# Kernel tuning notes

Hardware: AMD Instinct MI355X
Metric: run time of the kernel (lower is better)

The kernel has to match this reference:

```python
import jax, jax.numpy as jnp
import numpy as np

# ---- Cl(3,0) Cayley table: blade order [1, e1, e2, e3, e12, e13, e23, e123] ----
_IDX2BM = [0, 1, 2, 4, 3, 5, 6, 7]
_BM2IDX = {b: i for i, b in enumerate(_IDX2BM)}

def _blade_mul(i, j):
    a, b = _IDX2BM[i], _IDX2BM[j]
    s, aa = 0, a >> 1
    while aa:
        s += bin(aa & b).count('1')
        aa >>= 1
    return _BM2IDX[a ^ b], (-1) ** s

_pairs = [(i, j) + _blade_mul(i, j) for i in range(8) for j in range(8) if i != j]
_pairs = [(i, j, k, s) for (i, j, k, s) in _pairs if k != i and k != j]
SRC_I = np.array([p[0] for p in _pairs])  # (42,)
SRC_J = np.array([p[1] for p in _pairs])
TGT   = np.array([p[2] for p in _pairs])
SIGN  = np.array([p[3] for p in _pairs], dtype=np.float32)

ROPE_THETA = 10000.0


def _rope_tables(T, D, dtype):
    inv_freq = 1.0 / (ROPE_THETA ** (jnp.arange(0, D, 2, dtype=jnp.float32) / D))
    freqs = jnp.arange(T, dtype=jnp.float32)[:, None] * inv_freq[None, :]  # (T, D/2)
    emb = jnp.concatenate([freqs, freqs], axis=-1)  # (T, D)
    return jnp.cos(emb).astype(dtype), jnp.sin(emb).astype(dtype)


def _rotate_half(x):
    x1, x2 = jnp.split(x, 2, axis=-1)
    return jnp.concatenate([-x2, x1], axis=-1)


def setup_inputs() -> dict:
    key = jax.random.key(0)
    k1, k2, k3 = jax.random.split(key, 3)
    B, T, N, D = 2, 2048, 8, 128
    d_model = N * D
    mv = jax.random.normal(k1, (B, T, N, D), dtype=jnp.float32)
    # nn.Linear weights, stored as (in, out) for x @ W; scaled like default init
    W_qkv = jax.random.normal(k2, (d_model, 3 * d_model), dtype=jnp.float32) / np.sqrt(d_model)
    W_o = jax.random.normal(k3, (d_model, d_model), dtype=jnp.float32) / np.sqrt(d_model)
    alpha = jnp.ones((8, 8), dtype=jnp.float32) * 0.01  # cayley_mix_init_scale
    return {"mv": mv, "W_qkv": W_qkv, "W_o": W_o, "alpha": alpha}


def reference(mv, W_qkv, W_o, alpha):
    B, T, N, D = mv.shape
    x_flat = mv.reshape(B, T, N * D)
    qkv = (x_flat @ W_qkv).reshape(B, T, 3, N, D)
    q, k, v = qkv[:, :, 0], qkv[:, :, 1], qkv[:, :, 2]  # (B, T, N, D)

    cos, sin = _rope_tables(T, D, mv.dtype)  # (T, D)
    cos = cos[None, :, None, :]
    sin = sin[None, :, None, :]
    q = q * cos + _rotate_half(q) * sin
    k = k * cos + _rotate_half(k) * sin

    # (B, N, T, D)
    q = q.transpose(0, 2, 1, 3)
    k = k.transpose(0, 2, 1, 3)
    v = v.transpose(0, 2, 1, 3)

    scale = 1.0 / jnp.sqrt(jnp.asarray(D, dtype=mv.dtype))
    scores = jnp.einsum('bntd,bnsd->bnts', q, k) * scale  # (B, N, T, T)
    causal = jnp.tril(jnp.ones((T, T), dtype=bool))
    scores = jnp.where(causal[None, None], scores, -jnp.inf)
    attn = jax.nn.softmax(scores, axis=-1)
    out = jnp.einsum('bnts,bnsd->bntd', attn, v)  # (B, N, T, D)

    out = out.transpose(0, 2, 1, 3).reshape(B, T, N * D)
    out = (out @ W_o).reshape(B, T, N, D)

    # Cayley cross-blade mixing
    si, sj, tgt = jnp.asarray(SRC_I), jnp.asarray(SRC_J), jnp.asarray(TGT)
    pair_w = alpha[si, sj] * jnp.asarray(SIGN)  # (42,)
    contrib = out[:, :, si, :] * out[:, :, sj, :] * pair_w[None, None, :, None]
    mixed = jnp.zeros_like(out).at[:, :, tgt, :].add(contrib)
    return out + mixed
```

## Files before the change

kernel.cpp:

```cpp
#include <hip/hip_runtime.h>
#include <stdint.h>


typedef __attribute__((ext_vector_type(8)))  __bf16 bf16x8;
typedef __attribute__((ext_vector_type(4)))  float  f32x4;

__device__ __forceinline__ uint16_t f2bf(float f) {
    uint32_t u = __float_as_uint(f);
    u += 0x7FFFu + ((u >> 16) & 1u);
    return (uint16_t)(u >> 16);
}
__device__ __forceinline__ float bf2f(uint16_t h) {
    return __uint_as_float(((uint32_t)h) << 16);
}

__device__ __forceinline__ void gload_lds16(const void* g, void* l) {
    __builtin_amdgcn_global_load_lds(
        (__attribute__((address_space(1))) void*)g,
        (__attribute__((address_space(3))) void*)l, 16, 0, 0);
}

__global__ __launch_bounds__(256) void k_cast(const float* __restrict__ in,
                                              uint16_t* __restrict__ out, int n) {
    int i = blockIdx.x * 256 + threadIdx.x;
    if (i * 4 >= n) return;
    float4 v = ((const float4*)in)[i];
    ushort4 o = make_ushort4(f2bf(v.x), f2bf(v.y), f2bf(v.z), f2bf(v.w));
    ((ushort4*)out)[i] = o;
}

__global__ __launch_bounds__(256) void k_wtrans(const float* __restrict__ W,
                                                uint16_t* __restrict__ Wt,
                                                int K, int N) {
    __shared__ uint16_t tile[64][65];
    const int k0 = blockIdx.y * 64, n0 = blockIdx.x * 64;
    const int c = threadIdx.x & 63, r4 = threadIdx.x >> 6;
#pragma unroll
    for (int i = 0; i < 16; ++i) {
        int r = r4 + i * 4;
        tile[r][c] = f2bf(W[(size_t)(k0 + r) * N + n0 + c]);
    }
    __syncthreads();
#pragma unroll
    for (int i = 0; i < 16; ++i) {
        int r = r4 + i * 4;
        Wt[(size_t)(n0 + r) * K + k0 + c] = tile[c][r];
    }
}

__global__ __launch_bounds__(256) void k_tab(float* __restrict__ ct,
                                             float* __restrict__ st) {
    int i = blockIdx.x * 256 + threadIdx.x;
    int t = i >> 6, f = i & 63;
    float inv = expf(-(float)f * 0.14391156830441f);
    float ang = (float)t * inv;
    ct[i] = cosf(ang);
    st[i] = sinf(ang);
}

__global__ __launch_bounds__(256) void k_gemmqkv(const uint16_t* __restrict__ A,
                                                 const uint16_t* __restrict__ Bt,
                                                 const float* __restrict__ ct,
                                                 const float* __restrict__ st,
                                                 uint16_t* __restrict__ Qr,
                                                 uint16_t* __restrict__ Kr,
                                                 uint16_t* __restrict__ Vt) {
    __shared__ uint16_t Atile[128 * 32];
    __shared__ uint16_t Btile[128 * 32];
    __shared__ uint16_t Tl[128][132];
    const int lin = blockIdx.y * 24 + blockIdx.x;
    const int logical = (lin & 7) * 96 + (lin >> 3);
    const int bx = logical % 24;
    const int m0 = (logical / 24) << 7, n0 = bx << 7;
    const int sec = bx >> 3, head = bx & 7;
    const int tid = threadIdx.x;
    const int l = tid & 63, w = tid >> 6;
    const int lr = l & 15, lg = l >> 4;
    const int wm = (w >> 1) << 6, wn = (w & 1) << 6;
    const int K = 1024;

    f32x4 acc[4][4];
#pragma unroll
    for (int i = 0; i < 4; ++i)
#pragma unroll
        for (int j = 0; j < 4; ++j) acc[i][j] = (f32x4){0.f, 0.f, 0.f, 0.f};

    for (int kt = 0; kt < 32; ++kt) {
        const int k0 = kt << 5;
        __syncthreads();
#pragma unroll
        for (int c = 0; c < 4; ++c) {
            int idx = c * 256 + tid;
            if (idx < 512) {
                int r = idx >> 2, kc = (idx & 3) << 3;
                gload_lds16(A + (size_t)(m0 + r) * K + k0 + kc, &Atile[idx * 8]);
            } else {
                int i2 = idx - 512;
                int r = i2 >> 2, kc = (i2 & 3) << 3;
                gload_lds16(Bt + (size_t)(n0 + r) * K + k0 + kc, &Btile[i2 * 8]);
            }
        }
        __syncthreads();
        bf16x8 af[4], bfv[4];
#pragma unroll
        for (int i = 0; i < 4; ++i) {
            af[i]  = *(const bf16x8*)(&Atile[(wm + i * 16 + lr) * 32 + lg * 8]);
            bfv[i] = *(const bf16x8*)(&Btile[(wn + i * 16 + lr) * 32 + lg * 8]);
        }
#pragma unroll
        for (int mi = 0; mi < 4; ++mi)
#pragma unroll
            for (int ni = 0; ni < 4; ++ni)
                acc[mi][ni] = __builtin_amdgcn_mfma_f32_16x16x32_bf16(
                    af[mi], bfv[ni], acc[mi][ni], 0, 0, 0);
    }

    __syncthreads();
#pragma unroll
    for (int mi = 0; mi < 4; ++mi)
#pragma unroll
        for (int ni = 0; ni < 4; ++ni)
#pragma unroll
            for (int r = 0; r < 4; ++r)
                Tl[wm + mi * 16 + lg * 4 + r][wn + ni * 16 + lr] =
                    f2bf(acc[mi][ni][r]);
    __syncthreads();

    const int b = m0 >> 11, t0 = m0 & 2047;
    const size_t hidx = (size_t)(b * 8 + head);
    if (sec < 2) {
        uint16_t* outp = (sec == 0 ? Qr : Kr) + (hidx * 2048 + t0) * 128;
#pragma unroll
        for (int it = 0; it < 8; ++it) {
            int lin2 = it * 256 + tid;
            int tr = lin2 >> 4, d0 = (lin2 & 15) * 4;
            ushort4 lo = *(const ushort4*)&Tl[tr][d0];
            ushort4 hi = *(const ushort4*)&Tl[tr][d0 + 64];
            float4 cv = *(const float4*)&ct[(size_t)(t0 + tr) * 64 + d0];
            float4 sv = *(const float4*)&st[(size_t)(t0 + tr) * 64 + d0];
            ushort4 o1, o2;
            o1.x = f2bf(bf2f(lo.x) * cv.x - bf2f(hi.x) * sv.x);
            o2.x = f2bf(bf2f(hi.x) * cv.x + bf2f(lo.x) * sv.x);
            o1.y = f2bf(bf2f(lo.y) * cv.y - bf2f(hi.y) * sv.y);
            o2.y = f2bf(bf2f(hi.y) * cv.y + bf2f(lo.y) * sv.y);
            o1.z = f2bf(bf2f(lo.z) * cv.z - bf2f(hi.z) * sv.z);
            o2.z = f2bf(bf2f(hi.z) * cv.z + bf2f(lo.z) * sv.z);
            o1.w = f2bf(bf2f(lo.w) * cv.w - bf2f(hi.w) * sv.w);
            o2.w = f2bf(bf2f(hi.w) * cv.w + bf2f(lo.w) * sv.w);
            *(ushort4*)&outp[(size_t)tr * 128 + d0]      = o1;
            *(ushort4*)&outp[(size_t)tr * 128 + d0 + 64] = o2;
        }
    } else {
        uint16_t* vp = Vt + hidx * 128 * 2048;
#pragma unroll
        for (int it = 0; it < 8; ++it) {
            int lin2 = it * 256 + tid;
            int d = lin2 >> 4, tq = (lin2 & 15) * 8;
            ushort4 v0 = make_ushort4(Tl[tq + 0][d], Tl[tq + 1][d],
                                      Tl[tq + 2][d], Tl[tq + 3][d]);
            ushort4 v1 = make_ushort4(Tl[tq + 4][d], Tl[tq + 5][d],
                                      Tl[tq + 6][d], Tl[tq + 7][d]);
            *(ushort4*)&vp[(size_t)d * 2048 + t0 + tq]     = v0;
            *(ushort4*)&vp[(size_t)d * 2048 + t0 + tq + 4] = v1;
        }
    }
}

__global__ __launch_bounds__(256) void k_gemm2s(const uint16_t* __restrict__ A,
                                                const uint16_t* __restrict__ Bt,
                                                float* __restrict__ C) {
    __shared__ uint16_t Atile[128 * 32];
    __shared__ uint16_t Btile[64 * 32];
    const int kz = blockIdx.z;
    A  += (size_t)kz * 512;
    Bt += (size_t)kz * 512;
    C  += (size_t)kz * (4096u * 1024u);
    const int lin = blockIdx.y * 16 + blockIdx.x;
    const int logical = (lin & 7) * 64 + (lin >> 3);
    const int m0 = (logical >> 4) << 7, n0 = (logical & 15) << 6;
    const int tid = threadIdx.x;
    const int l = tid & 63, w = tid >> 6;
    const int lr = l & 15, lg = l >> 4;
    const int wm = (w >> 1) << 6, wn = (w & 1) << 5;

    f32x4 acc[4][2];
#pragma unroll
    for (int i = 0; i < 4; ++i)
#pragma unroll
        for (int j = 0; j < 2; ++j) acc[i][j] = (f32x4){0.f, 0.f, 0.f, 0.f};

    for (int kt = 0; kt < 16; ++kt) {
        const int k0 = kt << 5;
        __syncthreads();
#pragma unroll
        for (int c = 0; c < 3; ++c) {
            int idx = c * 256 + tid;
            if (idx < 512) {
                int r = idx >> 2, kc = (idx & 3) << 3;
                gload_lds16(A + (size_t)(m0 + r) * 1024 + k0 + kc, &Atile[idx * 8]);
            } else {
                int i2 = idx - 512;
                int r = i2 >> 2, kc = (i2 & 3) << 3;
                gload_lds16(Bt + (size_t)(n0 + r) * 1024 + k0 + kc, &Btile[i2 * 8]);
            }
        }
        __syncthreads();
        bf16x8 af[4], bfv[2];
#pragma unroll
        for (int i = 0; i < 4; ++i)
            af[i] = *(const bf16x8*)(&Atile[(wm + i * 16 + lr) * 32 + lg * 8]);
#pragma unroll
        for (int j = 0; j < 2; ++j)
            bfv[j] = *(const bf16x8*)(&Btile[(wn + j * 16 + lr) * 32 + lg * 8]);
#pragma unroll
        for (int mi = 0; mi < 4; ++mi)
#pragma unroll
            for (int ni = 0; ni < 2; ++ni)
                acc[mi][ni] = __builtin_amdgcn_mfma_f32_16x16x32_bf16(
                    af[mi], bfv[ni], acc[mi][ni], 0, 0, 0);
    }
#pragma unroll
    for (int mi = 0; mi < 4; ++mi)
#pragma unroll
        for (int ni = 0; ni < 2; ++ni)
#pragma unroll
            for (int r = 0; r < 4; ++r) {
                int row = m0 + wm + mi * 16 + lg * 4 + r;
                int col = n0 + wn + ni * 16 + lr;
                C[(size_t)row * 1024 + col] = acc[mi][ni][r];
            }
}

__global__ __launch_bounds__(256) void k_attn(const uint16_t* __restrict__ Qg,
                                              const uint16_t* __restrict__ Kg,
                                              const uint16_t* __restrict__ Vtg,
                                              uint16_t* __restrict__ AOg) {
    __shared__ uint16_t Klds[2][64 * 128];
    __shared__ uint16_t Vlds[2][128 * 64];
    __shared__ uint16_t Plds[4][16 * 64];

    const int bx = blockIdx.x;
    const int h  = bx & 15;
    const int t4 = (bx >> 4) & 15;
    const int qt = (bx < 256) ? (31 - t4) : t4;
    const int q0 = qt * 64;
    const int tid = threadIdx.x;
    const int l = tid & 63, w = tid >> 6;
    const int lr = l & 15, lg = l >> 4;
    const size_t headTD = (size_t)h * (2048 * 128);
    const uint16_t* Kh = Kg + headTD;
    const uint16_t* Vh = Vtg + headTD;

    bf16x8 qf[4];
    {
        const uint16_t* qp = Qg + headTD + (size_t)(q0 + w * 16 + lr) * 128 + lg * 8;
#pragma unroll
        for (int kc = 0; kc < 4; ++kc) qf[kc] = *(const bf16x8*)(qp + kc * 32);
    }

    f32x4 accO[8];
#pragma unroll
    for (int i = 0; i < 8; ++i) accO[i] = (f32x4){0.f, 0.f, 0.f, 0.f};
    float mrun = -1e30f, lrun = 0.f;

    const float SL2E = 0.08838834764831845f * 1.4426950408889634f;
    const int   swz  = (lr & 7) << 4;
    uint16_t* Pw = &Plds[w][0];

    auto STAGE = [&](int buf, int k0) {
#pragma unroll
        for (int p = 0; p < 4; ++p) {
            int u = p * 256 + tid;
            int row = u >> 4;
            int c16 = (u & 15) ^ (row & 7);
            gload_lds16(Kh + (size_t)(k0 + row) * 128 + c16 * 8,
                        (char*)&Klds[buf][0] + u * 16);
        }
#pragma unroll
        for (int p = 0; p < 4; ++p) {
            int u = p * 256 + tid;
            int d = u >> 3;
            int c8 = (u & 7) ^ (d & 7);
            gload_lds16(Vh + (size_t)d * 2048 + k0 + c8 * 8,
                        (char*)&Vlds[buf][0] + u * 16);
        }
    };

    STAGE(0, 0);

    for (int kt = 0; kt <= qt; ++kt) {
        asm volatile("s_waitcnt vmcnt(0)" ::: "memory");
        __builtin_amdgcn_s_barrier();
        __builtin_amdgcn_sched_barrier(0);
        if (kt < qt) STAGE((kt + 1) & 1, (kt + 1) * 64);

        const char* Kb = (const char*)&Klds[kt & 1][0];
        const char* Vb = (const char*)&Vlds[kt & 1][0];

        float sv[4][4];
        __builtin_amdgcn_s_setprio(1);
#pragma unroll
        for (int cg = 0; cg < 4; ++cg) {
            f32x4 a = (f32x4){0.f, 0.f, 0.f, 0.f};
#pragma unroll
            for (int kc = 0; kc < 4; ++kc) {
                int kb = (cg * 16 + lr) * 256 + ((kc * 64 + lg * 16) ^ swz);
                bf16x8 kf = *(const bf16x8*)(Kb + kb);
                a = __builtin_amdgcn_mfma_f32_16x16x32_bf16(kf, qf[kc], a, 0, 0, 0);
            }
#pragma unroll
            for (int r = 0; r < 4; ++r) sv[cg][r] = a[r];
        }
        __builtin_amdgcn_s_setprio(0);

        if (kt == qt) {
#pragma unroll
            for (int cg = 0; cg < 4; ++cg)
#pragma unroll
                for (int r = 0; r < 4; ++r)
                    if (cg * 16 + lg * 4 + r > w * 16 + lr) sv[cg][r] = -1e30f;
        }

        float pml = sv[0][0];
#pragma unroll
        for (int cg = 0; cg < 4; ++cg)
#pragma unroll
            for (int r = 0; r < 4; ++r) pml = fmaxf(pml, sv[cg][r]);

        if (!__all(pml * SL2E <= mrun + 11.f)) {
            float mx = pml;
            mx = fmaxf(mx, __shfl_xor(mx, 16, 64));
            mx = fmaxf(mx, __shfl_xor(mx, 32, 64));
            float mn = fmaxf(mrun, mx * SL2E);
            float corr = exp2f(mrun - mn);
            mrun = mn;
            lrun *= corr;
            float ca[4];
#pragma unroll
            for (int r = 0; r < 4; ++r)
                ca[r] = __shfl(corr, (lg << 4) + lg * 4 + r, 64);
#pragma unroll
            for (int i = 0; i < 8; ++i)
#pragma unroll
                for (int r = 0; r < 4; ++r) accO[i][r] *= ca[r];
        }

        float psum = 0.f;
        float p[4][4];
#pragma unroll
        for (int cg = 0; cg < 4; ++cg)
#pragma unroll
            for (int r = 0; r < 4; ++r) {
                p[cg][r] = exp2f(fmaf(sv[cg][r], SL2E, -mrun));
                psum += p[cg][r];
            }
        lrun += psum;

#pragma unroll
        for (int cg = 0; cg < 4; ++cg) {
            uint32_t w0, w1;
            asm("v_cvt_pk_bf16_f32 %0, %1, %2" : "=v"(w0) : "v"(p[cg][0]), "v"(p[cg][1]));
            asm("v_cvt_pk_bf16_f32 %0, %1, %2" : "=v"(w1) : "v"(p[cg][2]), "v"(p[cg][3]));
            uint2 pr; pr.x = w0; pr.y = w1;
            *(uint2*)((char*)Pw + lr * 128 + ((cg * 32 + lg * 8) ^ swz)) = pr;
        }

        asm volatile("" ::: "memory");
        bf16x8 pf[2];
#pragma unroll
        for (int c = 0; c < 2; ++c)
            pf[c] = *(const bf16x8*)((char*)Pw + lr * 128 + ((c * 64 + lg * 16) ^ swz));

        __builtin_amdgcn_s_setprio(1);
#pragma unroll
        for (int ni = 0; ni < 8; ++ni)
#pragma unroll
            for (int c = 0; c < 2; ++c) {
                int vb = (ni * 16 + lr) * 128 + ((c * 64 + lg * 16) ^ swz);
                bf16x8 vf = *(const bf16x8*)(Vb + vb);
                accO[ni] = __builtin_amdgcn_mfma_f32_16x16x32_bf16(pf[c], vf, accO[ni], 0, 0, 0);
            }
        __builtin_amdgcn_s_setprio(0);
    }

    float lsum = lrun;
    lsum += __shfl_xor(lsum, 16, 64);
    lsum += __shfl_xor(lsum, 32, 64);
    float linv = 1.f / lsum;
    float inv[4];
#pragma unroll
    for (int r = 0; r < 4; ++r)
        inv[r] = __shfl(linv, (lg << 4) + lg * 4 + r, 64);
    const int b = h >> 3, n = h & 7;
#pragma unroll
    for (int ni = 0; ni < 8; ++ni)
#pragma unroll
        for (int r = 0; r < 4; ++r) {
            int trow = q0 + w * 16 + lg * 4 + r;
            AOg[((size_t)(b * 2048 + trow)) * 1024 + n * 128 + ni * 16 + lr] =
                f2bf(accO[ni][r] * inv[r]);
        }
}

__global__ __launch_bounds__(256) void k_mix(const float* __restrict__ out0,
                                             const float* __restrict__ out1,
                                             const float* __restrict__ alpha,
                                             float* __restrict__ fin) {
    constexpr int SI[42] = {1,1,1,1,1,1, 2,2,2,2,2,2, 3,3,3,3,3,3, 4,4,4,4,4,4,
                            5,5,5,5,5,5, 6,6,6,6,6,6, 7,7,7,7,7,7};
    constexpr int SJ[42] = {2,3,4,5,6,7, 1,3,4,5,6,7, 1,2,4,5,6,7, 1,2,3,5,6,7,
                            1,2,3,4,6,7, 1,2,3,4,5,7, 1,2,3,4,5,6};
    constexpr int TG[42] = {4,5,2,3,7,6, 4,6,1,7,3,5, 5,6,7,1,2,4, 2,1,7,6,5,3,
                            3,7,1,6,4,2, 7,3,2,5,4,1, 6,5,4,3,2,1};
    constexpr float SG[42] = {+1,+1,+1,+1,+1,+1, -1,+1,-1,-1,+1,-1, -1,-1,+1,-1,-1,+1,
                              -1,+1,+1,-1,+1,-1, -1,-1,+1,+1,-1,+1, +1,-1,+1,-1,+1,-1,
                              +1,-1,+1,-1,+1,-1};
    int idx = blockIdx.x * 256 + threadIdx.x;
    int dq = (idx & 31) * 4, bt = idx >> 5;
    size_t base = (size_t)bt * 1024 + dq;
    float4 o[8], r[8];
#pragma unroll
    for (int hh = 0; hh < 8; ++hh) {
        float4 a = *(const float4*)&out0[base + hh * 128];
        float4 b = *(const float4*)&out1[base + hh * 128];
        o[hh] = make_float4(a.x + b.x, a.y + b.y, a.z + b.z, a.w + b.w);
        r[hh] = o[hh];
    }
#pragma unroll
    for (int p = 0; p < 42; ++p) {
        float wgt = alpha[SI[p] * 8 + SJ[p]] * SG[p];
        r[TG[p]].x += wgt * o[SI[p]].x * o[SJ[p]].x;
        r[TG[p]].y += wgt * o[SI[p]].y * o[SJ[p]].y;
        r[TG[p]].z += wgt * o[SI[p]].z * o[SJ[p]].z;
        r[TG[p]].w += wgt * o[SI[p]].w * o[SJ[p]].w;
    }
#pragma unroll
    for (int hh = 0; hh < 8; ++hh) *(float4*)&fin[base + hh * 128] = r[hh];
}

extern "C" void kernel_launch(void* const* d_in, const int* in_sizes, int n_in,
                              void* d_out, int out_size, void* d_ws, size_t ws_size,
                              hipStream_t stream) {
    (void)in_sizes; (void)n_in; (void)out_size; (void)ws_size;
    const float* mv    = (const float*)d_in[0];
    const float* Wqkv  = (const float*)d_in[1];
    const float* Wo    = (const float*)d_in[2];
    const float* alpha = (const float*)d_in[3];
    float* outp = (float*)d_out;
    char* ws = (char*)d_ws;

    uint16_t* Xbf  = (uint16_t*)(ws + 0);
    uint16_t* Wqt  = (uint16_t*)(ws + 8388608);
    uint16_t* Wot  = (uint16_t*)(ws + 14680064);
    uint16_t* Qr   = (uint16_t*)(ws + 41943040);
    uint16_t* Kr   = (uint16_t*)(ws + 50331648);
    uint16_t* Vt   = (uint16_t*)(ws + 58720256);
    float*    ctab = (float*)(ws + 67108864);
    float*    stab = (float*)(ws + 67633152);
    uint16_t* AO   = (uint16_t*)(ws + 0);
    float*    outF0 = (float*)(ws + 16777216);
    float*    outF1 = (float*)(ws + 33554432);

    k_cast   <<<4096, 256, 0, stream>>>(mv, Xbf, 4096 * 1024);
    k_wtrans <<<dim3(48, 16), 256, 0, stream>>>(Wqkv, Wqt, 1024, 3072);
    k_wtrans <<<dim3(16, 16), 256, 0, stream>>>(Wo, Wot, 1024, 1024);
    k_tab    <<<512, 256, 0, stream>>>(ctab, stab);
    k_gemmqkv<<<dim3(24, 32), 256, 0, stream>>>(Xbf, Wqt, ctab, stab, Qr, Kr, Vt);
    k_attn   <<<512, 256, 0, stream>>>(Qr, Kr, Vt, AO);
    k_gemm2s <<<dim3(16, 32, 2), 256, 0, stream>>>(AO, Wot, outF0);
    k_mix    <<<512, 256, 0, stream>>>(outF0, outF1, alpha, outp);
}
```

Measured before the change: 133.9 us.

## Merge prep kernels and use 64-wide XOR-swizzled K tiles in GEMMs

Fuses the cast, the two weight transposes and the RoPE table kernels into one launch to cut launch overhead. Both GEMMs now stage K tiles of 64 with an XOR swizzle on 16-byte chunks, which halves the number of barrier and load rounds and avoids LDS bank conflicts on fragment reads. The QKV GEMM aliases its epilogue transpose buffer onto the operand tiles to keep LDS use the same. Larger tiles raise LDS use per block in gemm2s, which may lower occupancy.

Measured after the change: 121.5 us. -9.3%, faster.

```diff
diff --git a/kernel.cpp b/kernel.cpp
--- a/kernel.cpp
+++ b/kernel.cpp
@@ -20,42 +20,48 @@
         (__attribute__((address_space(3))) void*)l, 16, 0, 0);
 }
 
-__global__ __launch_bounds__(256) void k_cast(const float* __restrict__ in,
-                                              uint16_t* __restrict__ out, int n) {
-    int i = blockIdx.x * 256 + threadIdx.x;
-    if (i * 4 >= n) return;
-    float4 v = ((const float4*)in)[i];
-    ushort4 o = make_ushort4(f2bf(v.x), f2bf(v.y), f2bf(v.z), f2bf(v.w));
-    ((ushort4*)out)[i] = o;
-}
-
-__global__ __launch_bounds__(256) void k_wtrans(const float* __restrict__ W,
-                                                uint16_t* __restrict__ Wt,
-                                                int K, int N) {
+__global__ __launch_bounds__(256) void k_prep(const float* __restrict__ mv,
+                                              const float* __restrict__ Wqkv,
+                                              const float* __restrict__ Wo,
+                                              uint16_t* __restrict__ Xbf,
+                                              uint16_t* __restrict__ Wqt,
+                                              uint16_t* __restrict__ Wot,
+                                              float* __restrict__ ct,
+                                              float* __restrict__ st) {
     __shared__ uint16_t tile[64][65];
-    const int k0 = blockIdx.y * 64, n0 = blockIdx.x * 64;
-    const int c = threadIdx.x & 63, r4 = threadIdx.x >> 6;
-#pragma unroll
-    for (int i = 0; i < 16; ++i) {
-        int r = r4 + i * 4;
-        tile[r][c] = f2bf(W[(size_t)(k0 + r) * N + n0 + c]);
-    }
-    __syncthreads();
-#pragma unroll
-    for (int i = 0; i < 16; ++i) {
-        int r = r4 + i * 4;
-        Wt[(size_t)(n0 + r) * K + k0 + c] = tile[c][r];
-    }
-}
-
-__global__ __launch_bounds__(256) void k_tab(float* __restrict__ ct,
-                                             float* __restrict__ st) {
-    int i = blockIdx.x * 256 + threadIdx.x;
-    int t = i >> 6, f = i & 63;
-    float inv = expf(-(float)f * 0.14391156830441f);
-    float ang = (float)t * inv;
-    ct[i] = cosf(ang);
-    st[i] = sinf(ang);
+    const int bid = blockIdx.x;
+    const int tid = threadIdx.x;
+    if (bid < 4096) {
+        int i = bid * 256 + tid;
+        float4 v = ((const float4*)mv)[i];
+        ((ushort4*)Xbf)[i] = make_ushort4(f2bf(v.x), f2bf(v.y), f2bf(v.z), f2bf(v.w));
+    } else if (bid < 5120) {
+        const float* W; uint16_t* Wt; int N, bx, by;
+        if (bid < 4864) { W = Wqkv; Wt = Wqt; N = 3072;
+                          int b2 = bid - 4096; bx = b2 % 48; by = b2 / 48; }
+        else            { W = Wo;   Wt = Wot; N = 1024;
+                          int b3 = bid - 4864; bx = b3 & 15; by = b3 >> 4; }
+        const int k0 = by * 64, n0 = bx * 64;
+        const int c = tid & 63, r4 = tid >> 6;
+#pragma unroll
+        for (int i = 0; i < 16; ++i) {
+            int r = r4 + i * 4;
+            tile[r][c] = f2bf(W[(size_t)(k0 + r) * N + n0 + c]);
+        }
+        __syncthreads();
+#pragma unroll
+        for (int i = 0; i < 16; ++i) {
+            int r = r4 + i * 4;
+            Wt[(size_t)(n0 + r) * 1024 + k0 + c] = tile[c][r];
+        }
+    } else {
+        int i = (bid - 5120) * 256 + tid;
+        int t = i >> 6, f = i & 63;
+        float inv = expf(-(float)f * 0.14391156830441f);
+        float ang = (float)t * inv;
+        ct[i] = cosf(ang);
+        st[i] = sinf(ang);
+    }
 }
 
 __global__ __launch_bounds__(256) void k_gemmqkv(const uint16_t* __restrict__ A,
@@ -65,9 +71,9 @@
                                                  uint16_t* __restrict__ Qr,
                                                  uint16_t* __restrict__ Kr,
                                                  uint16_t* __restrict__ Vt) {
-    __shared__ uint16_t Atile[128 * 32];
-    __shared__ uint16_t Btile[128 * 32];
-    __shared__ uint16_t Tl[128][132];
+    __shared__ __align__(16) char smem[33792];
+    uint16_t* Atile = (uint16_t*)smem;
+    uint16_t* Btile = (uint16_t*)(smem + 16384);
     const int lin = blockIdx.y * 24 + blockIdx.x;
     const int logical = (lin & 7) * 96 + (lin >> 3);
     const int bx = logical % 24;
@@ -85,37 +91,47 @@
 #pragma unroll
         for (int j = 0; j < 4; ++j) acc[i][j] = (f32x4){0.f, 0.f, 0.f, 0.f};
 
-    for (int kt = 0; kt < 32; ++kt) {
-        const int k0 = kt << 5;
+    for (int kt = 0; kt < 16; ++kt) {
+        const int k0 = kt << 6;
         __syncthreads();
 #pragma unroll
-        for (int c = 0; c < 4; ++c) {
+        for (int c = 0; c < 8; ++c) {
             int idx = c * 256 + tid;
-            if (idx < 512) {
-                int r = idx >> 2, kc = (idx & 3) << 3;
-                gload_lds16(A + (size_t)(m0 + r) * K + k0 + kc, &Atile[idx * 8]);
+            if (idx < 1024) {
+                int r = idx >> 3, c16 = idx & 7;
+                int sc = c16 ^ (r & 7);
+                gload_lds16(A + (size_t)(m0 + r) * K + k0 + sc * 8, Atile + idx * 8);
             } else {
-                int i2 = idx - 512;
-                int r = i2 >> 2, kc = (i2 & 3) << 3;
-                gload_lds16(Bt + (size_t)(n0 + r) * K + k0 + kc, &Btile[i2 * 8]);
+                int i2 = idx - 1024;
+                int r = i2 >> 3, c16 = i2 & 7;
+                int sc = c16 ^ (r & 7);
+                gload_lds16(Bt + (size_t)(n0 + r) * K + k0 + sc * 8, Btile + i2 * 8);
             }
         }
         __syncthreads();
-        bf16x8 af[4], bfv[4];
-#pragma unroll
-        for (int i = 0; i < 4; ++i) {
-            af[i]  = *(const bf16x8*)(&Atile[(wm + i * 16 + lr) * 32 + lg * 8]);
-            bfv[i] = *(const bf16x8*)(&Btile[(wn + i * 16 + lr) * 32 + lg * 8]);
-        }
-#pragma unroll
-        for (int mi = 0; mi < 4; ++mi)
-#pragma unroll
-            for (int ni = 0; ni < 4; ++ni)
-                acc[mi][ni] = __builtin_amdgcn_mfma_f32_16x16x32_bf16(
-                    af[mi], bfv[ni], acc[mi][ni], 0, 0, 0);
+#pragma unroll
+        for (int kk = 0; kk < 2; ++kk) {
+            bf16x8 af[4], bfv[4];
+#pragma unroll
+            for (int i = 0; i < 4; ++i) {
+                int ra = wm + i * 16 + lr;
+                af[i]  = *(const bf16x8*)((char*)Atile + ra * 128 +
+                          ((kk * 64 + lg * 16) ^ ((ra & 7) << 4)));
+                int rb = wn + i * 16 + lr;
+                bfv[i] = *(const bf16x8*)((char*)Btile + rb * 128 +
+                          ((kk * 64 + lg * 16) ^ ((rb & 7) << 4)));
+            }
+#pragma unroll
+            for (int mi = 0; mi < 4; ++mi)
+#pragma unroll
+                for (int ni = 0; ni < 4; ++ni)
+                    acc[mi][ni] = __builtin_amdgcn_mfma_f32_16x16x32_bf16(
+                        af[mi], bfv[ni], acc[mi][ni], 0, 0, 0);
+        }
     }
 
     __syncthreads();
+    uint16_t (*Tl)[132] = (uint16_t(*)[132])smem;
 #pragma unroll
     for (int mi = 0; mi < 4; ++mi)
 #pragma unroll
@@ -169,8 +185,8 @@
 __global__ __launch_bounds__(256) void k_gemm2s(const uint16_t* __restrict__ A,
                                                 const uint16_t* __restrict__ Bt,
                                                 float* __restrict__ C) {
-    __shared__ uint16_t Atile[128 * 32];
-    __shared__ uint16_t Btile[64 * 32];
+    __shared__ uint16_t Atile[128 * 64];
+    __shared__ uint16_t Btile[64 * 64];
     const int kz = blockIdx.z;
     A  += (size_t)kz * 512;
     Bt += (size_t)kz * 512;
@@ -189,35 +205,46 @@
 #pragma unroll
         for (int j = 0; j < 2; ++j) acc[i][j] = (f32x4){0.f, 0.f, 0.f, 0.f};
 
-    for (int kt = 0; kt < 16; ++kt) {
-        const int k0 = kt << 5;
+    for (int kt = 0; kt < 8; ++kt) {
+        const int k0 = kt << 6;
         __syncthreads();
 #pragma unroll
-        for (int c = 0; c < 3; ++c) {
+        for (int c = 0; c < 6; ++c) {
             int idx = c * 256 + tid;
-            if (idx < 512) {
-                int r = idx >> 2, kc = (idx & 3) << 3;
-                gload_lds16(A + (size_t)(m0 + r) * 1024 + k0 + kc, &Atile[idx * 8]);
+            if (idx < 1024) {
+                int r = idx >> 3, c16 = idx & 7;
+                int sc = c16 ^ (r & 7);
+                gload_lds16(A + (size_t)(m0 + r) * 1024 + k0 + sc * 8, Atile + idx * 8);
             } else {
-                int i2 = idx - 512;
-                int r = i2 >> 2, kc = (i2 & 3) << 3;
-                gload_lds16(Bt + (size_t)(n0 + r) * 1024 + k0 + kc, &Btile[i2 * 8]);
+                int i2 = idx - 1024;
+                int r = i2 >> 3, c16 = i2 & 7;
+                int sc = c16 ^ (r & 7);
+                gload_lds16(Bt + (size_t)(n0 + r) * 1024 + k0 + sc * 8, Btile + i2 * 8);
             }
         }
         __syncthreads();
-        bf16x8 af[4], bfv[2];
-#pragma unroll
-        for (int i = 0; i < 4; ++i)
-            af[i] = *(const bf16x8*)(&Atile[(wm + i * 16 + lr) * 32 + lg * 8]);
-#pragma unroll
-        for (int j = 0; j < 2; ++j)
-            bfv[j] = *(const bf16x8*)(&Btile[(wn + j * 16 + lr) * 32 + lg * 8]);
-#pragma unroll
-        for (int mi = 0; mi < 4; ++mi)
-#pragma unroll
-            for (int ni = 0; ni < 2; ++ni)
-                acc[mi][ni] = __builtin_amdgcn_mfma_f32_16x16x32_bf16(
-                    af[mi], bfv[ni], acc[mi][ni], 0, 0, 0);
+#pragma unroll
+        for (int kk = 0; kk < 2; ++kk) {
+            bf16x8 af[4], bfv[2];
+#pragma unroll
+            for (int i = 0; i < 4; ++i) {
+                int ra = wm + i * 16 + lr;
+                af[i] = *(const bf16x8*)((char*)Atile + ra * 128 +
+                         ((kk * 64 + lg * 16) ^ ((ra & 7) << 4)));
+            }
+#pragma unroll
+            for (int j = 0; j < 2; ++j) {
+                int rb = wn + j * 16 + lr;
+                bfv[j] = *(const bf16x8*)((char*)Btile + rb * 128 +
+                          ((kk * 64 + lg * 16) ^ ((rb & 7) << 4)));
+            }
+#pragma unroll
+            for (int mi = 0; mi < 4; ++mi)
+#pragma unroll
+                for (int ni = 0; ni < 2; ++ni)
+                    acc[mi][ni] = __builtin_amdgcn_mfma_f32_16x16x32_bf16(
+                        af[mi], bfv[ni], acc[mi][ni], 0, 0, 0);
+        }
     }
 #pragma unroll
     for (int mi = 0; mi < 4; ++mi)
@@ -461,10 +488,7 @@
     float*    outF0 = (float*)(ws + 16777216);
     float*    outF1 = (float*)(ws + 33554432);
 
-    k_cast   <<<4096, 256, 0, stream>>>(mv, Xbf, 4096 * 1024);
-    k_wtrans <<<dim3(48, 16), 256, 0, stream>>>(Wqkv, Wqt, 1024, 3072);
-    k_wtrans <<<dim3(16, 16), 256, 0, stream>>>(Wo, Wot, 1024, 1024);
-    k_tab    <<<512, 256, 0, stream>>>(ctab, stab);
+    k_prep   <<<5632, 256, 0, stream>>>(mv, Wqkv, Wo, Xbf, Wqt, Wot, ctab, stab);
     k_gemmqkv<<<dim3(24, 32), 256, 0, stream>>>(Xbf, Wqt, ctab, stab, Qr, Kr, Vt);
     k_attn   <<<512, 256, 0, stream>>>(Qr, Kr, Vt, AO);
     k_gemm2s <<<dim3(16, 32, 2), 256, 0, stream>>>(AO, Wot, outF0);
```
